# Kernel tuning notes

Measured on AMD Instinct MI355X. Metric: run time of the kernel, lower is better.

## Reference

```python
import jax, jax.numpy as jnp
import numpy as np

B, S, N, E = 16, 2048, 256, 4096      # batch, tokens, max entities, edges per sample
H, LD, ETR = 512, 16, 768             # hidden_size, label_emb_dim, transformer dim
D = H + LD                            # graph_dim = 528
C1 = 3                                # num_edge_classes + 1
GL = 2                                # gcn_layers
NLBL = 15                             # num_node_classes + 2


def setup_inputs() -> dict:
    key = jax.random.key(0)
    ks = jax.random.split(key, 14)
    s = 0.02
    inp = {}
    inp["emb"] = jax.random.normal(ks[0], (B, S, ETR), jnp.float32)
    inp["ent_indices"] = jax.random.randint(ks[1], (B, S), 0, N + 1)
    inp["ent_labels"] = jax.random.randint(ks[2], (B, N), 0, NLBL)
    inp["edge_index"] = jax.random.randint(ks[3], (B, 2, E), 0, N + 1)
    inp["edge_attr"] = jax.random.randint(ks[4], (B, E), 0, C1)
    inp["cands"] = jax.random.randint(ks[5], (B, N + 1, N + 1), 0, 2).astype(bool)
    inp["W_red"] = jax.random.normal(ks[6], (ETR, H), jnp.float32) * s
    inp["b_red"] = jnp.zeros((H,), jnp.float32)
    inp["emb_label_tbl"] = jax.random.normal(ks[7], (NLBL, LD), jnp.float32) * s
    inp["W_gcn"] = jax.random.normal(ks[8], (C1, GL, D, D), jnp.float32) * s
    inp["b_gcn"] = jnp.zeros((C1, GL, D), jnp.float32)
    inp["W_head"] = jax.random.normal(ks[9], (D, D), jnp.float32) * s
    inp["b_head"] = jnp.zeros((D,), jnp.float32)
    inp["W_tail"] = jax.random.normal(ks[10], (D, D), jnp.float32) * s
    inp["b_tail"] = jnp.zeros((D,), jnp.float32)
    inp["W_out"] = jax.random.normal(ks[11], (D, C1), jnp.float32) * s
    inp["b_out"] = jnp.zeros((C1,), jnp.float32)
    return inp


def _gcn_layer(x, src, dst, w_e, W, b):
    """PyG GCNConv with edge weights w_e (0/1 relation mask) and self loops.
    x: [n, D]; src/dst: [E]; aggregation flow source->target."""
    n = x.shape[0]
    h = x @ W
    deg = jax.ops.segment_sum(w_e, dst, num_segments=n) + 1.0  # +1 self loop
    dinv = jax.lax.rsqrt(deg)
    coef = w_e * dinv[src] * dinv[dst]                         # D^-1/2 A D^-1/2
    agg = jax.ops.segment_sum(coef[:, None] * h[src], dst, num_segments=n)
    return agg + h / deg[:, None] + b                          # self-loop norm = 1/deg


def reference(emb, ent_indices, ent_labels, edge_index, edge_attr, cands,
              W_red, b_red, emb_label_tbl, W_gcn, b_gcn,
              W_head, b_head, W_tail, b_tail, W_out, b_out):
    n_nodes = cands.shape[1]  # max_num_ent + 1
    # fc_reduction of frozen transformer embeddings
    red = emb @ W_red + b_red                                   # [B,S,H]
    # tag-based segment aggregation: max over (mask * emb) == max(segment_max, 0)
    seg_max = jax.vmap(lambda e, ids: jax.ops.segment_max(e, ids, num_segments=n_nodes))(red, ent_indices)
    ent_hidden = jnp.maximum(seg_max, 0.0).at[:, 0, :].set(0.0)  # tag 0 stays zero
    # label embeddings: tag t uses ent_labels[:, t-1]; zeroed where label==0
    lab = emb_label_tbl[ent_labels] * (ent_labels != 0)[..., None].astype(red.dtype)
    lab0 = jnp.broadcast_to(emb_label_tbl[0], (lab.shape[0], 1, lab.shape[-1]))
    label_part = jnp.concatenate([lab0, lab], axis=1)           # [B,n_nodes,LD]
    x0 = jnp.concatenate([label_part, ent_hidden], axis=-1)     # [B,n_nodes,D]
    # multi-relation GCN: per edge class, stacked GCNConv, summed then averaged
    src, dst = edge_index[:, 0], edge_index[:, 1]
    layer_v = jax.vmap(_gcn_layer, in_axes=(0, 0, 0, 0, None, None))
    result = jnp.zeros_like(x0)
    n_cls = W_gcn.shape[0]
    for c in range(n_cls):
        w_e = (edge_attr == c).astype(x0.dtype)
        x = x0
        for l in range(W_gcn.shape[1]):
            x = layer_v(x, src, dst, w_e, W_gcn[c, l], b_gcn[c, l])
        result = result + x
    result = result / n_cls
    # head/tail projections and 'add' pairwise features gated by candidate mask
    x_head = result @ W_head + b_head
    x_tail = result @ W_tail + b_tail
    m = cands[:, :, 1:].astype(x0.dtype)                        # [B,n_nodes,n_nodes-1]
    # fc_out is linear: ((h_i + t_j) * m_ij) @ W + b == m_ij*(hW_i + tW_j) + b
    hW = x_head @ W_out                                         # [B,n_nodes,C1]
    tW = x_tail[:, 1:] @ W_out                                  # [B,n_nodes-1,C1]
    logits = (hW[:, :, None, :] + tW[:, None, :, :]) * m[..., None] + b_out
    return logits  # [B, n_nodes, n_nodes-1, C1] edge-class logits
```

## Files before the change

kernel.cpp:

```cpp
#include <hip/hip_runtime.h>
#include <hip/hip_bf16.h>

typedef unsigned short u16;
typedef __attribute__((ext_vector_type(8))) short short8;
typedef __attribute__((ext_vector_type(4))) float floatx4;

#define B_ 16
#define S_ 2048
#define NNODE 257
#define E_ 4096
#define ETR_ 768
#define H_ 512
#define D_ 528
#define KPAD 544
#define NC 3
#define NROW (B_*NNODE)
#define DD (D_*D_)

#define BM 128
#define BN 128
#define BK 32

__device__ inline u16 f2b(float x) {
    __hip_bfloat16 h = __float2bfloat16(x);
    return *(u16*)&h;
}
__device__ inline float b2f(u16 u) {
    return __uint_as_float(((unsigned)u) << 16);
}
__device__ inline float b2f_lo(unsigned v) { return __uint_as_float(v << 16); }
__device__ inline float b2f_hi(unsigned v) { return __uint_as_float(v & 0xffff0000u); }

__device__ inline void gll16(const u16* g, u16* l) {
    __builtin_amdgcn_global_load_lds(
        (const __attribute__((address_space(1))) void*)g,
        (__attribute__((address_space(3))) void*)l,
        16, 0, 0);
}

__device__ inline int clampi(int v, int hi) { return v < hi ? v : hi; }

__device__ inline void exscan_lds(int* cnt, int n, int tid, int* wsums)
{
    const int lane = tid & 63, wave = tid >> 6;
    int v[4];
    int ts = 0;
#pragma unroll
    for (int j = 0; j < 4; j++) {
        const int i = tid * 4 + j;
        v[j] = (i < n) ? cnt[i] : 0;
        ts += v[j];
    }
    int inc = ts;
#pragma unroll
    for (int off = 1; off < 64; off <<= 1) {
        const int o = __shfl_up(inc, off, 64);
        if (lane >= off) inc += o;
    }
    if (lane == 63) wsums[wave] = inc;
    __syncthreads();
    int woff = 0;
#pragma unroll
    for (int w = 0; w < 4; w++) if (w < wave) woff += wsums[w];
    int run = woff + inc - ts;
#pragma unroll
    for (int j = 0; j < 4; j++) {
        const int i = tid * 4 + j;
        if (i < n) { const int c = v[j]; cnt[i] = run; run += c; }
    }
}

__global__ void cvt_bf16(const float* __restrict__ in, u16* __restrict__ out, int n4)
{
    const int i = blockIdx.x * 256 + threadIdx.x;
    if (i < n4) {
        const float4 f = ((const float4*)in)[i];
        ushort4 o;
        o.x = f2b(f.x); o.y = f2b(f.y); o.z = f2b(f.z); o.w = f2b(f.w);
        ((ushort4*)out)[i] = o;
    }
}

__global__ void transpose_cvt(const float* __restrict__ in, u16* __restrict__ out,
                              int R, int Cc, size_t instride, size_t outstride,
                              int opitch)
{
    __shared__ float t[32][33];
    const int z = blockIdx.z;
    const int tx = threadIdx.x & 31, ty = threadIdx.x >> 5;
    const int c0 = blockIdx.x * 32, r0 = blockIdx.y * 32;
    const float* ip = in + z * instride;
    u16* op = out + z * outstride;
#pragma unroll
    for (int i = 0; i < 4; i++) {
        const int r = r0 + ty + i * 8, c = c0 + tx;
        if (r < R && c < Cc) t[ty + i * 8][tx] = ip[(size_t)r * Cc + c];
    }
    __syncthreads();
#pragma unroll
    for (int i = 0; i < 4; i++) {
        const int c = c0 + ty + i * 8, r = r0 + tx;
        if (c < Cc && r < opitch) {
            const u16 val = (r < R) ? f2b(t[tx][ty + i * 8]) : (u16)0;
            op[(size_t)c * opitch + r] = val;
        }
    }
}

template<int SWZ, int OB16>
__global__ __launch_bounds__(256)
void gemm_mfma(const u16* __restrict__ A, const u16* __restrict__ Wt,
               const float* __restrict__ bias_base, size_t bias_stride,
               void* __restrict__ Cv, int M, int N, int K, float scale,
               size_t astride, size_t wstride, size_t cstride, int cpitch)
{
    __shared__ u16 SS[16384];
    const int tid = threadIdx.x;
    const int wave = tid >> 6, lane = tid & 63;
    const int quad = lane >> 4, l16 = lane & 15;
    const int z = blockIdx.z;
    int bx = blockIdx.x, by = blockIdx.y;
    if (SWZ) {
        const int lin = blockIdx.x + (blockIdx.y << 2);
        bx = (lin >> 3) & 3;
        by = (lin & 7) + ((lin >> 5) << 3);
    }
    const int m0 = by * BM, n0 = bx * BN;

    floatx4 acc[2][8];
#pragma unroll
    for (int t = 0; t < 2; t++)
#pragma unroll
        for (int u = 0; u < 8; u++)
#pragma unroll
            for (int r = 0; r < 4; r++) acc[t][u][r] = 0.f;

    const int srow = tid >> 2;
    const int scol = (((tid & 3) ^ ((srow >> 1) & 3))) * 8;
    const u16* aP0 = A + z * astride + (size_t)clampi(m0 + srow,      M - 1) * K + scol;
    const u16* aP1 = A + z * astride + (size_t)clampi(m0 + 64 + srow, M - 1) * K + scol;
    const u16* bP0 = Wt + z * wstride + (size_t)clampi(n0 + srow,      N - 1) * K + scol;
    const u16* bP1 = Wt + z * wstride + (size_t)clampi(n0 + 64 + srow, N - 1) * K + scol;
    const int lsw = wave * 512;

    const int sw8 = ((l16 >> 1) & 3) * 8;

    {
        u16* d = &SS[lsw];
        gll16(aP0, d);
        gll16(aP1, d + 2048);
        gll16(bP0, d + 4096);
        gll16(bP1, d + 6144);
    }
    __syncthreads();

    const int nt = K / BK;
    int cur = 0;
    for (int t = 0; t < nt; ++t) {
        if (t + 1 < nt) {
            const int kn = (t + 1) * BK;
            u16* d = &SS[(cur ^ 1) * 8192 + lsw];
            gll16(aP0 + kn, d);
            gll16(aP1 + kn, d + 2048);
            gll16(bP0 + kn, d + 4096);
            gll16(bP1 + kn, d + 6144);
        }
        const u16* Sb = &SS[cur * 8192];
        short8 af[2], bfv[8];
        af[0] = *(const short8*)&Sb[(wave * 32 + l16) * 32 + ((quad * 8) ^ sw8)];
        af[1] = *(const short8*)&Sb[(wave * 32 + 16 + l16) * 32 + ((quad * 8) ^ sw8)];
#pragma unroll
        for (int u = 0; u < 8; u++)
            bfv[u] = *(const short8*)&Sb[4096 + (u * 16 + l16) * 32 + ((quad * 8) ^ sw8)];
#pragma unroll
        for (int t2 = 0; t2 < 2; t2++)
#pragma unroll
            for (int u = 0; u < 8; u++)
                acc[t2][u] = __builtin_amdgcn_mfma_f32_16x16x32_bf16(af[t2], bfv[u], acc[t2][u], 0, 0, 0);
        __syncthreads();
        cur ^= 1;
    }

    const float* bias = bias_base ? (bias_base + z * bias_stride) : nullptr;
#pragma unroll
    for (int t = 0; t < 2; t++) {
#pragma unroll
        for (int r = 0; r < 4; r++) {
            const int m = m0 + wave * 32 + t * 16 + quad * 4 + r;
            if (m >= M) continue;
#pragma unroll
            for (int u = 0; u < 8; u++) {
                const int n = n0 + u * 16 + l16;
                if (n < N) {
                    const float v = acc[t][u][r] * scale + (bias ? bias[n] : 0.f);
                    if (OB16) {
                        u16* Cb = (u16*)Cv;
                        Cb[z * cstride + (size_t)m * cpitch + n] = f2b(v);
                    } else {
                        float* Cf = (float*)Cv;
                        Cf[z * cstride + (size_t)m * cpitch + n] = v;
                    }
                }
            }
        }
    }
}

template<int MODE>
__global__ __launch_bounds__(256)
void gemm64(const float* __restrict__ A, const float* __restrict__ W,
            const float* __restrict__ bias, float* __restrict__ C,
            int M, int N, int K, float scale,
            const int* __restrict__ segidx, float* __restrict__ segout)
{
    __shared__ float Asl[16][68];
    __shared__ float Bsl[16][64];
    const int tid = threadIdx.x;
    const int tx = tid & 15, ty = tid >> 4;
    const int m0 = blockIdx.y * 64, n0 = blockIdx.x * 64;
    const int arow = tid >> 2, acol = (tid & 3) * 4;
    const int brow = tid >> 4, bcol = (tid & 15) * 4;

    float acc[4][4];
#pragma unroll
    for (int i = 0; i < 4; i++)
#pragma unroll
        for (int j = 0; j < 4; j++) acc[i][j] = 0.f;

    for (int kk = 0; kk < K; kk += 16) {
        float4 av = make_float4(0.f, 0.f, 0.f, 0.f);
        if (m0 + arow < M) av = *(const float4*)(A + (size_t)(m0 + arow) * K + kk + acol);
        Asl[acol + 0][arow] = av.x; Asl[acol + 1][arow] = av.y;
        Asl[acol + 2][arow] = av.z; Asl[acol + 3][arow] = av.w;
        float4 bv = make_float4(0.f, 0.f, 0.f, 0.f);
        if (n0 + bcol < N) bv = *(const float4*)(W + (size_t)(kk + brow) * N + n0 + bcol);
        *(float4*)&Bsl[brow][bcol] = bv;
        __syncthreads();
#pragma unroll
        for (int k = 0; k < 16; k++) {
            const float4 a = *(const float4*)&Asl[k][ty * 4];
            const float4 b = *(const float4*)&Bsl[k][tx * 4];
            const float af[4] = { a.x, a.y, a.z, a.w };
            const float bfv[4] = { b.x, b.y, b.z, b.w };
#pragma unroll
            for (int i = 0; i < 4; i++)
#pragma unroll
                for (int j = 0; j < 4; j++) acc[i][j] += af[i] * bfv[j];
        }
        __syncthreads();
    }

#pragma unroll
    for (int i = 0; i < 4; i++) {
        const int m = m0 + ty * 4 + i;
        if (m >= M) continue;
        if (MODE == 1) {
            const int bb = m >> 11;
            const int idx = segidx[m];
            float* const srow = segout + (((size_t)bb * NNODE + idx) << 9);
#pragma unroll
            for (int j = 0; j < 4; j++) {
                const int n = n0 + tx * 4 + j;
                const float v = acc[i][j] + (bias ? bias[n] : 0.f);
                atomicMax(((int*)srow) + n, __float_as_int(v));
            }
        } else {
#pragma unroll
            for (int j = 0; j < 4; j++) {
                const int n = n0 + tx * 4 + j;
                if (n < N) {
                    const float v = acc[i][j] * scale + (bias ? bias[n] : 0.f);
                    C[(size_t)m * N + n] = v;
                }
            }
        }
    }
}

__global__ void csr_all(const int* __restrict__ ent_indices,
                        int* __restrict__ rptr, int* __restrict__ rlist,
                        const int* __restrict__ edge_index, const int* __restrict__ edge_attr,
                        float* __restrict__ degf, int* __restrict__ csr_ptr,
                        int2* __restrict__ csr_sc)
{
    __shared__ int cnt[NC * NNODE];
    __shared__ float dinvl[NC * NNODE];
    __shared__ int wsums[4];
    const int b = blockIdx.x;
    const int tid = threadIdx.x;

    const int* idx = ent_indices + (size_t)b * S_;
    for (int i = tid; i < NNODE; i += 256) cnt[i] = 0;
    __syncthreads();
    for (int r = tid; r < S_; r += 256) atomicAdd(&cnt[idx[r]], 1);
    __syncthreads();
    exscan_lds(cnt, NNODE, tid, wsums);
    __syncthreads();
    for (int i = tid; i < NNODE; i += 256) rptr[b * (NNODE + 1) + i] = cnt[i];
    if (tid == 0) rptr[b * (NNODE + 1) + NNODE] = S_;
    __syncthreads();
    for (int r = tid; r < S_; r += 256) {
        const int pos = atomicAdd(&cnt[idx[r]], 1);
        rlist[(size_t)b * S_ + pos] = r;
    }
    __syncthreads();

    const int* src = edge_index + (size_t)b * 2 * E_;
    const int* dst = src + E_;
    const int* attr = edge_attr + (size_t)b * E_;
    for (int i = tid; i < NC * NNODE; i += 256) cnt[i] = 0;
    __syncthreads();
    for (int e = tid; e < E_; e += 256) atomicAdd(&cnt[attr[e] * NNODE + dst[e]], 1);
    __syncthreads();
    for (int i = tid; i < NC * NNODE; i += 256) {
        const float d = (float)cnt[i] + 1.0f;
        degf[(size_t)b * NC * NNODE + i] = d;
        dinvl[i] = rsqrtf(d);
    }
    __syncthreads();
    exscan_lds(cnt, NC * NNODE, tid, wsums);
    __syncthreads();
    for (int i = tid; i < NC * NNODE; i += 256) csr_ptr[(size_t)b * NC * NNODE + i] = cnt[i];
    __syncthreads();
    for (int e = tid; e < E_; e += 256) {
        const int a = attr[e], d = dst[e], s = src[e];
        const int pos = atomicAdd(&cnt[a * NNODE + d], 1);
        const float cf = dinvl[a * NNODE + s] * dinvl[a * NNODE + d];
        csr_sc[(size_t)b * E_ + pos] = make_int2(s, __float_as_int(cf));
    }
}

__global__ __launch_bounds__(256)
void segmax_x0(const u16* __restrict__ redC, const int* __restrict__ rptr,
               const int* __restrict__ rlist, const float* __restrict__ b_red,
               const int* __restrict__ ent_labels, const float* __restrict__ tbl,
               u16* __restrict__ x0b)
{
    const int bn = blockIdx.x;
    const int b = bn / NNODE, n = bn % NNODE;
    const int tid = threadIdx.x;
    const int c0 = tid * 2;
    const int start = rptr[b * (NNODE + 1) + n];
    const int end   = (n == 0) ? start : rptr[b * (NNODE + 1) + n + 1];
    float m0 = -INFINITY, m1 = -INFINITY;
    const int* rl = rlist + (size_t)b * S_;
    int nr = (start < end) ? rl[start] : 0;
    for (int i = start; i < end; i++) {
        const int r = nr;
        if (i + 1 < end) nr = rl[i + 1];
        const u16* row = redC + ((size_t)b * S_ + r) * H_;
        const unsigned v = *(const unsigned*)(row + c0);
        m0 = fmaxf(m0, b2f_lo(v & 0xffffu));
        m1 = fmaxf(m1, b2f_hi(v));
    }
    float h0, h1;
    if (n == 0) { h0 = 0.f; h1 = 0.f; }
    else {
        h0 = fmaxf(m0 + b_red[c0], 0.f);
        h1 = fmaxf(m1 + b_red[c0 + 1], 0.f);
    }
    u16* orow = x0b + (size_t)bn * KPAD;
    *(unsigned*)(orow + 16 + c0) = (unsigned)f2b(h0) | ((unsigned)f2b(h1) << 16);
    if (tid < 16) {
        float v;
        if (n == 0) v = tbl[tid];
        else {
            const int lab = ent_labels[b * (NNODE - 1) + (n - 1)];
            v = (lab != 0) ? tbl[lab * 16 + tid] : 0.f;
        }
        orow[tid] = f2b(v);
    } else if (tid < 32) {
        orow[512 + tid] = 0;
    }
}

template<int OUTB>
__global__ void build_x0(const float* __restrict__ seg, const int* __restrict__ ent_labels,
                         const float* __restrict__ tbl, float* __restrict__ x0f,
                         u16* __restrict__ x0b)
{
    const int bn = blockIdx.x;
    const int b = bn / NNODE, n = bn % NNODE;
    const int CMAX = OUTB ? KPAD : D_;
    for (int col = threadIdx.x; col < CMAX; col += blockDim.x) {
        float v;
        if (col >= D_) {
            v = 0.f;
        } else if (col < 16) {
            if (n == 0) v = tbl[col];
            else {
                const int lab = ent_labels[b * (NNODE - 1) + (n - 1)];
                v = (lab != 0) ? tbl[lab * 16 + col] : 0.f;
            }
        } else {
            v = (n == 0) ? 0.f : seg[(((size_t)b * NNODE + n) << 9) + (col - 16)];
        }
        if (OUTB) x0b[(size_t)bn * KPAD + col] = f2b(v);
        else      x0f[(size_t)bn * D_ + col] = v;
    }
}

template<int OUT>
__global__ __launch_bounds__(256)
void gcn_gather(const u16* __restrict__ h, size_t hstride,
                const float* __restrict__ degf,
                const int* __restrict__ csr_ptr, const int2* __restrict__ csr_sc,
                const float* __restrict__ bias_base, size_t bias_stride,
                float* __restrict__ outf, u16* __restrict__ outb, size_t ostride)
{
    const int bn = blockIdx.x;
    const int cls = blockIdx.y;
    const int b = bn / NNODE, n = bn % NNODE;
    const int tid = threadIdx.x;
    const int base = b * NC * NNODE + cls * NNODE + n;
    const float d = degf[base];
    const int start = csr_ptr[base];
    const int cnt = (int)d - 1;
    const float inv = 1.0f / d;
    const u16* hp = h + cls * hstride;
    const float* bias = bias_base + cls * bias_stride;
    const u16* hrow = hp + (size_t)bn * KPAD;
    const int c0 = 2 * tid;
    const int c1 = 512 + 2 * tid;
    const bool hi = (tid < 8);
    unsigned v = *(const unsigned*)(hrow + c0);
    float a0 = b2f_lo(v & 0xffffu) * inv + bias[c0];
    float a1 = b2f_hi(v) * inv + bias[c0 + 1];
    float a2 = 0.f, a3 = 0.f;
    if (hi) {
        v = *(const unsigned*)(hrow + c1);
        a2 = b2f_lo(v & 0xffffu) * inv + bias[c1];
        a3 = b2f_hi(v) * inv + bias[c1 + 1];
    }
    const int2* scp = csr_sc + (size_t)b * E_ + start;
    int2 sc = (cnt > 0) ? scp[0] : make_int2(0, 0);
    for (int i = 0; i < cnt; i++) {
        const int2 cur = sc;
        if (i + 1 < cnt) sc = scp[i + 1];
        const float cf = __int_as_float(cur.y);
        const u16* hs = hp + ((size_t)b * NNODE + cur.x) * KPAD;
        v = *(const unsigned*)(hs + c0);
        a0 += cf * b2f_lo(v & 0xffffu);
        a1 += cf * b2f_hi(v);
        if (hi) {
            v = *(const unsigned*)(hs + c1);
            a2 += cf * b2f_lo(v & 0xffffu);
            a3 += cf * b2f_hi(v);
        }
    }
    if (OUT == 0) {
        u16* orow = outb + cls * ostride + (size_t)bn * KPAD;
        *(unsigned*)(orow + c0) = (unsigned)f2b(a0) | ((unsigned)f2b(a1) << 16);
        if (hi) *(unsigned*)(orow + c1) = (unsigned)f2b(a2) | ((unsigned)f2b(a3) << 16);
        if (tid >= 8 && tid < 16)
            *(unsigned*)(orow + 528 + 2 * (tid - 8)) = 0;
    } else {
        float* orow = outf + cls * ostride + (size_t)bn * D_;
        orow[c0] = a0; orow[c0 + 1] = a1;
        if (hi) { orow[c1] = a2; orow[c1 + 1] = a3; }
    }
}

template<int OUT>
__global__ __launch_bounds__(256)
void gcn_gather_f32(const float* __restrict__ h, size_t hstride,
                    const float* __restrict__ degf,
                    const int* __restrict__ csr_ptr, const int2* __restrict__ csr_sc,
                    const float* __restrict__ bias_base, size_t bias_stride,
                    float* __restrict__ outf, int cls0)
{
    const int bn = blockIdx.x;
    const int cls = cls0 + blockIdx.y;
    const int b = bn / NNODE, n = bn % NNODE;
    const int tid = threadIdx.x;
    const int base = b * NC * NNODE + cls * NNODE + n;
    const float d = degf[base];
    const int start = csr_ptr[base];
    const int cnt = (int)d - 1;
    const float inv = 1.0f / d;
    const float* hp = h + blockIdx.y * hstride;
    const float* bias = bias_base + cls * bias_stride;
    const float* hrow = hp + (size_t)bn * D_;
    const int c0 = tid, c1 = tid + 256, c2 = tid + 512;
    float a0 = hrow[c0] * inv + bias[c0];
    float a1 = hrow[c1] * inv + bias[c1];
    float a2 = (c2 < D_) ? hrow[c2] * inv + bias[c2] : 0.f;
    const int2* scp = csr_sc + (size_t)b * E_ + start;
    for (int i = 0; i < cnt; i++) {
        const int2 sc = scp[i];
        const float cf = __int_as_float(sc.y);
        const float* hs = hp + ((size_t)b * NNODE + sc.x) * D_;
        a0 += cf * hs[c0];
        a1 += cf * hs[c1];
        if (c2 < D_) a2 += cf * hs[c2];
    }
    if (OUT == 1) {
        float* orow = outf + (size_t)bn * D_;
        orow[c0] += a0; orow[c1] += a1; if (c2 < D_) orow[c2] += a2;
    } else {
        float* orow = outf + (size_t)bn * D_;
        orow[c0] = a0; orow[c1] = a1; if (c2 < D_) orow[c2] = a2;
    }
}

__global__ void rowdot3(const float* __restrict__ x, const float* __restrict__ w,
                        float* __restrict__ out)
{
    const int row = blockIdx.x;
    const int lane = threadIdx.x;
    float a0 = 0.f, a1 = 0.f, a2 = 0.f;
    for (int d = lane; d < D_; d += 64) {
        const float xv = x[(size_t)row * D_ + d];
        a0 += xv * w[d * 3 + 0];
        a1 += xv * w[d * 3 + 1];
        a2 += xv * w[d * 3 + 2];
    }
#pragma unroll
    for (int off = 32; off > 0; off >>= 1) {
        a0 += __shfl_down(a0, off, 64);
        a1 += __shfl_down(a1, off, 64);
        a2 += __shfl_down(a2, off, 64);
    }
    if (lane == 0) {
        out[(size_t)row * 3 + 0] = a0;
        out[(size_t)row * 3 + 1] = a1;
        out[(size_t)row * 3 + 2] = a2;
    }
}

__global__ void prep_heads(const float* __restrict__ W_head, const float* __restrict__ W_tail,
                           const float* __restrict__ b_head, const float* __restrict__ b_tail,
                           const float* __restrict__ W_out,
                           float* __restrict__ Whw, float* __restrict__ Wtw,
                           float* __restrict__ bias6)
{
    const int r = blockIdx.x;
    const int lane = threadIdx.x;
    const float* x; float* o;
    if (r < D_)            { x = W_head + (size_t)r * D_;        o = Whw + (size_t)r * 3; }
    else if (r < 2 * D_)   { x = W_tail + (size_t)(r - D_) * D_; o = Wtw + (size_t)(r - D_) * 3; }
    else if (r == 2 * D_)  { x = b_head;                         o = bias6; }
    else                   { x = b_tail;                         o = bias6 + 3; }
    float a0 = 0.f, a1 = 0.f, a2 = 0.f;
    for (int d = lane; d < D_; d += 64) {
        const float xv = x[d];
        a0 += xv * W_out[d * 3 + 0];
        a1 += xv * W_out[d * 3 + 1];
        a2 += xv * W_out[d * 3 + 2];
    }
#pragma unroll
    for (int off = 32; off > 0; off >>= 1) {
        a0 += __shfl_down(a0, off, 64);
        a1 += __shfl_down(a1, off, 64);
        a2 += __shfl_down(a2, off, 64);
    }
    if (lane == 0) { o[0] = a0; o[1] = a1; o[2] = a2; }
}

__global__ __launch_bounds__(256)
void rowdot6(const float* __restrict__ x3, size_t zstride,
             const float* __restrict__ Whw, const float* __restrict__ Wtw,
             const float* __restrict__ bias6,
             float* __restrict__ hw, float* __restrict__ tw)
{
    const int row = blockIdx.x * 4 + (threadIdx.x >> 6);
    const int lane = threadIdx.x & 63;
    const float* p0 = x3 + (size_t)row * D_;
    const float* p1 = p0 + zstride;
    const float* p2 = p1 + zstride;
    float h0 = 0.f, h1 = 0.f, h2 = 0.f, t0 = 0.f, t1 = 0.f, t2 = 0.f;
    for (int d = lane; d < D_; d += 64) {
        const float xv = (p0[d] + p1[d] + p2[d]) * (1.f / 3.f);
        h0 += xv * Whw[d * 3 + 0]; h1 += xv * Whw[d * 3 + 1]; h2 += xv * Whw[d * 3 + 2];
        t0 += xv * Wtw[d * 3 + 0]; t1 += xv * Wtw[d * 3 + 1]; t2 += xv * Wtw[d * 3 + 2];
    }
#pragma unroll
    for (int off = 32; off > 0; off >>= 1) {
        h0 += __shfl_down(h0, off, 64); h1 += __shfl_down(h1, off, 64); h2 += __shfl_down(h2, off, 64);
        t0 += __shfl_down(t0, off, 64); t1 += __shfl_down(t1, off, 64); t2 += __shfl_down(t2, off, 64);
    }
    if (lane == 0) {
        hw[(size_t)row * 3 + 0] = h0 + bias6[0];
        hw[(size_t)row * 3 + 1] = h1 + bias6[1];
        hw[(size_t)row * 3 + 2] = h2 + bias6[2];
        tw[(size_t)row * 3 + 0] = t0 + bias6[3];
        tw[(size_t)row * 3 + 1] = t1 + bias6[4];
        tw[(size_t)row * 3 + 2] = t2 + bias6[5];
    }
}

__global__ __launch_bounds__(256)
void final_logits(const float* __restrict__ hw, const float* __restrict__ tw,
                  const int* __restrict__ cands, const float* __restrict__ b_out,
                  float* __restrict__ out)
{
    const int bi = blockIdx.x;
    const int b = bi / NNODE;
    const int j = threadIdx.x;
    const float h0 = hw[bi * 3 + 0], h1 = hw[bi * 3 + 1], h2 = hw[bi * 3 + 2];
    const int tj = b * NNODE + 1 + j;
    const float t0 = tw[tj * 3 + 0], t1 = tw[tj * 3 + 1], t2 = tw[tj * 3 + 2];
    const float m = (cands[(size_t)bi * NNODE + 1 + j] != 0) ? 1.f : 0.f;
    const float bo0 = b_out[0], bo1 = b_out[1], bo2 = b_out[2];
    const size_t o = ((size_t)bi * 256 + j) * 3;
    out[o + 0] = (h0 + t0) * m + bo0;
    out[o + 1] = (h1 + t1) * m + bo1;
    out[o + 2] = (h2 + t2) * m + bo2;
}

extern "C" void kernel_launch(void* const* d_in, const int* in_sizes, int n_in,
                              void* d_out, int out_size, void* d_ws, size_t ws_size,
                              hipStream_t stream)
{
    const float* emb       = (const float*)d_in[0];
    const int* ent_indices = (const int*)d_in[1];
    const int* ent_labels  = (const int*)d_in[2];
    const int* edge_index  = (const int*)d_in[3];
    const int* edge_attr   = (const int*)d_in[4];
    const int* cands       = (const int*)d_in[5];
    const float* W_red     = (const float*)d_in[6];
    const float* b_red     = (const float*)d_in[7];
    const float* tbl       = (const float*)d_in[8];
    const float* W_gcn     = (const float*)d_in[9];
    const float* b_gcn     = (const float*)d_in[10];
    const float* W_head    = (const float*)d_in[11];
    const float* b_head    = (const float*)d_in[12];
    const float* W_tail    = (const float*)d_in[13];
    const float* b_tail    = (const float*)d_in[14];
    const float* W_out     = (const float*)d_in[15];
    const float* b_out     = (const float*)d_in[16];

    char* ws = (char*)d_ws;
    size_t off = 0;
    auto alloc = [&](size_t nbytes) -> char* {
        char* p = ws + off; off = (off + nbytes + 255) & ~(size_t)255; return p;
    };
    const size_t ROWB  = (size_t)NROW * D_ * sizeof(float);
    const size_t RD    = (size_t)NROW * D_;
    const size_t RD2   = (size_t)NROW * KPAD;
    const size_t WGZ   = (size_t)2 * D_ * KPAD;

    char* R0      = alloc((size_t)B_ * S_ * ETR_ * sizeof(u16));
    u16*  emb_bf  = (u16*)R0;
    u16*  hbB     = (u16*)R0;
    u16*  x1b     = (u16*)(R0 + (size_t)16 * 1024 * 1024);
    char* R1      = alloc((size_t)B_ * S_ * H_ * sizeof(u16));
    u16*  redC    = (u16*)R1;
    float* result3 = (float*)R1;
    int*  rptr    = (int*)alloc((size_t)B_ * (NNODE + 1) * 4);
    int*  rlist   = (int*)alloc((size_t)B_ * S_ * 4);
    u16*  x0b     = (u16*)alloc((size_t)NROW * KPAD * sizeof(u16));
    u16*  wredT   = (u16*)alloc((size_t)H_ * ETR_ * sizeof(u16));
    u16*  wgcnT   = (u16*)alloc((size_t)NC * WGZ * sizeof(u16));
    float* Whw    = (float*)alloc((size_t)D_ * 3 * 4);
    float* Wtw    = (float*)alloc((size_t)D_ * 3 * 4);
    float* bias6  = (float*)alloc(6 * 4);
    float* degf   = (float*)alloc((size_t)B_ * NC * NNODE * 4);
    float* hwp    = (float*)alloc((size_t)NROW * 3 * 4);
    float* twp    = (float*)alloc((size_t)NROW * 3 * 4);
    int* csr_ptr  = (int*)alloc((size_t)B_ * NC * NNODE * 4);
    int2* csr_sc  = (int2*)alloc((size_t)B_ * E_ * 8);
    const bool fast = (ws_size >= off);

    if (fast) {
        const int n4e = (B_ * S_ * ETR_) / 4;
        cvt_bf16<<<(n4e + 255) / 256, 256, 0, stream>>>(emb, emb_bf, n4e);
        transpose_cvt<<<dim3(16, 24, 1), 256, 0, stream>>>(W_red, wredT, ETR_, H_, 0, 0, ETR_);
        transpose_cvt<<<dim3(17, 17, 6), 256, 0, stream>>>(W_gcn, wgcnT, D_, D_, DD, (size_t)D_ * KPAD, KPAD);

        prep_heads<<<2 * D_ + 2, 64, 0, stream>>>(W_head, W_tail, b_head, b_tail, W_out,
                                                  Whw, Wtw, bias6);

        csr_all<<<B_, 256, 0, stream>>>(ent_indices, rptr, rlist,
                                        edge_index, edge_attr, degf, csr_ptr, csr_sc);

        gemm_mfma<1, 1><<<dim3(H_ / BN, (B_ * S_) / BM, 1), 256, 0, stream>>>(
            emb_bf, wredT, nullptr, 0, redC, B_ * S_, H_, ETR_, 1.f, 0, 0, 0, H_);
        segmax_x0<<<B_ * NNODE, 256, 0, stream>>>(redC, rptr, rlist, b_red,
                                                  ent_labels, tbl, x0b);

        dim3 gmm((D_ + BN - 1) / BN, (NROW + BM - 1) / BM, NC);
        gemm_mfma<0, 1><<<gmm, 256, 0, stream>>>(
            x0b, wgcnT, nullptr, 0, hbB, NROW, D_, KPAD, 1.f, 0, WGZ, RD2, KPAD);
        gcn_gather<0><<<dim3(NROW, NC), 256, 0, stream>>>(
            hbB, RD2, degf, csr_ptr, csr_sc, b_gcn, (size_t)2 * D_,
            nullptr, x1b, RD2);
        gemm_mfma<0, 1><<<gmm, 256, 0, stream>>>(
            x1b, wgcnT + (size_t)D_ * KPAD, nullptr, 0, hbB, NROW, D_, KPAD, 1.f,
            RD2, WGZ, RD2, KPAD);
        gcn_gather<2><<<dim3(NROW, NC), 256, 0, stream>>>(
            hbB, RD2, degf, csr_ptr, csr_sc, b_gcn + D_, (size_t)2 * D_,
            result3, nullptr, RD);

        rowdot6<<<NROW / 4, 256, 0, stream>>>(result3, RD, Whw, Wtw, bias6, hwp, twp);
        final_logits<<<NROW, 256, 0, stream>>>(hwp, twp, cands, b_out, (float*)d_out);
        return;
    }

    off = 0;
    float* bufA = (float*)alloc(ROWB);
    float* bufB = (float*)alloc(ROWB);
    float* bufC = (float*)alloc(ROWB);
    float* bufD = (float*)alloc(ROWB);
    degf = (float*)alloc((size_t)B_ * NC * NNODE * 4);
    hwp  = (float*)alloc((size_t)NROW * 3 * 4);
    twp  = (float*)alloc((size_t)NROW * 3 * 4);
    csr_ptr = (int*)alloc((size_t)B_ * NC * NNODE * 4);
    csr_sc  = (int2*)alloc((size_t)B_ * E_ * 8);
    int* rptr2  = (int*)alloc((size_t)B_ * (NNODE + 1) * 4);
    int* rlist2 = (int*)alloc((size_t)B_ * S_ * 4);

    hipMemsetAsync(bufA, 0, (size_t)B_ * NNODE * H_ * 4, stream);
    hipMemsetAsync(bufD, 0, ROWB, stream);
    gemm64<1><<<dim3(H_ / 64, (B_ * S_) / 64), 256, 0, stream>>>(
        emb, W_red, b_red, nullptr, B_ * S_, H_, ETR_, 1.f, ent_indices, bufA);
    build_x0<0><<<NROW, 256, 0, stream>>>(bufA, ent_labels, tbl, bufB, nullptr);
    csr_all<<<B_, 256, 0, stream>>>(ent_indices, rptr2, rlist2,
                                    edge_index, edge_attr, degf, csr_ptr, csr_sc);
    dim3 gridG((D_ + 63) / 64, (NROW + 63) / 64);
    for (int c = 0; c < NC; c++) {
        gemm64<0><<<gridG, 256, 0, stream>>>(bufB, W_gcn + (size_t)(c * 2 + 0) * DD,
            nullptr, bufA, NROW, D_, D_, 1.f, nullptr, nullptr);
        gcn_gather_f32<2><<<dim3(NROW, 1), 256, 0, stream>>>(bufA, 0, degf, csr_ptr, csr_sc,
            b_gcn, (size_t)2 * D_, bufC, c);
        gemm64<0><<<gridG, 256, 0, stream>>>(bufC, W_gcn + (size_t)(c * 2 + 1) * DD,
            nullptr, bufA, NROW, D_, D_, 1.f, nullptr, nullptr);
        gcn_gather_f32<1><<<dim3(NROW, 1), 256, 0, stream>>>(bufA, 0, degf, csr_ptr, csr_sc,
            b_gcn + D_, (size_t)2 * D_, bufD, c);
    }
    gemm64<0><<<gridG, 256, 0, stream>>>(bufD, W_head, b_head, bufB,
        NROW, D_, D_, 1.f / 3.f, nullptr, nullptr);
    gemm64<0><<<gridG, 256, 0, stream>>>(bufD, W_tail, b_tail, bufC,
        NROW, D_, D_, 1.f / 3.f, nullptr, nullptr);
    rowdot3<<<NROW, 64, 0, stream>>>(bufB, W_out, hwp);
    rowdot3<<<NROW, 64, 0, stream>>>(bufC, W_out, twp);
    final_logits<<<NROW, 256, 0, stream>>>(hwp, twp, cands, b_out, (float*)d_out);
}
```

Baseline: 400.1 us.

## Triple-buffer GEMM shared memory with prefetch distance two and explicit waitcnts

Moves the MFMA GEMM from double to triple buffering in LDS. Two K-tiles are prefetched ahead, and explicit vmcnt and lgkmcnt waits with raw barriers replace the __syncthreads at the end of each iteration. The aim is to hide global-to-LDS load latency better and cut stalls at barriers. In exchange, LDS per block grows, which may reduce occupancy, and correctness now depends on the hand-written waitcnt counts.

Result: no change. 396.2 us (-1.0%).

```diff
diff --git a/kernel.cpp b/kernel.cpp
--- a/kernel.cpp
+++ b/kernel.cpp
@@ -114,7 +114,7 @@
                void* __restrict__ Cv, int M, int N, int K, float scale,
                size_t astride, size_t wstride, size_t cstride, int cpitch)
 {
-    __shared__ u16 SS[16384];
+    __shared__ u16 SS[24576];
     const int tid = threadIdx.x;
     const int wave = tid >> 6, lane = tid & 63;
     const int quad = lane >> 4, l16 = lane & 15;
@@ -145,26 +145,26 @@
 
     const int sw8 = ((l16 >> 1) & 3) * 8;
 
+    const int nt = K / BK;
+
     {
         u16* d = &SS[lsw];
-        gll16(aP0, d);
-        gll16(aP1, d + 2048);
-        gll16(bP0, d + 4096);
-        gll16(bP1, d + 6144);
-    }
-    __syncthreads();
-
-    const int nt = K / BK;
+        gll16(aP0, d); gll16(aP1, d + 2048);
+        gll16(bP0, d + 4096); gll16(bP1, d + 6144);
+    }
+    if (nt > 1) {
+        const int k1 = BK;
+        u16* d = &SS[8192 + lsw];
+        gll16(aP0 + k1, d); gll16(aP1 + k1, d + 2048);
+        gll16(bP0 + k1, d + 4096); gll16(bP1 + k1, d + 6144);
+    }
+
     int cur = 0;
     for (int t = 0; t < nt; ++t) {
-        if (t + 1 < nt) {
-            const int kn = (t + 1) * BK;
-            u16* d = &SS[(cur ^ 1) * 8192 + lsw];
-            gll16(aP0 + kn, d);
-            gll16(aP1 + kn, d + 2048);
-            gll16(bP0 + kn, d + 4096);
-            gll16(bP1 + kn, d + 6144);
-        }
+        if (t + 1 < nt) asm volatile("s_waitcnt vmcnt(4)" ::: "memory");
+        else            asm volatile("s_waitcnt vmcnt(0)" ::: "memory");
+        __builtin_amdgcn_s_barrier();
+
         const u16* Sb = &SS[cur * 8192];
         short8 af[2], bfv[8];
         af[0] = *(const short8*)&Sb[(wave * 32 + l16) * 32 + ((quad * 8) ^ sw8)];
@@ -172,13 +172,25 @@
 #pragma unroll
         for (int u = 0; u < 8; u++)
             bfv[u] = *(const short8*)&Sb[4096 + (u * 16 + l16) * 32 + ((quad * 8) ^ sw8)];
+        asm volatile("s_waitcnt lgkmcnt(0)" ::: "memory");
+        __builtin_amdgcn_sched_barrier(0);
+        __builtin_amdgcn_s_barrier();
+
+        if (t + 2 < nt) {
+            int s = cur + 2; if (s >= 3) s -= 3;
+            const int kn = (t + 2) * BK;
+            u16* d = &SS[s * 8192 + lsw];
+            gll16(aP0 + kn, d); gll16(aP1 + kn, d + 2048);
+            gll16(bP0 + kn, d + 4096); gll16(bP1 + kn, d + 6144);
+        }
+
 #pragma unroll
         for (int t2 = 0; t2 < 2; t2++)
 #pragma unroll
             for (int u = 0; u < 8; u++)
                 acc[t2][u] = __builtin_amdgcn_mfma_f32_16x16x32_bf16(af[t2], bfv[u], acc[t2][u], 0, 0, 0);
-        __syncthreads();
-        cur ^= 1;
+
+        cur = (cur == 2) ? 0 : cur + 1;
     }
 
     const float* bias = bias_base ? (bias_base + z * bias_stride) : nullptr;
```
